# Kernel optimization log

Measured on AMD Instinct MI355X. Metric: run time of the kernel, lower is better.

Reference implementation:

```python
import jax, jax.numpy as jnp
import numpy as np

COMMIT = 0.25
DECAY = 0.999
EPS = 1e-05


def setup_inputs() -> dict:
    key = jax.random.key(0)
    k1, k2, k3, k4 = jax.random.split(key, 4)
    N, M, D = 8, 512, 32
    B, H, W = 32, 32, 32
    return {
        "x": jax.random.normal(k1, (B, N * D, H, W), jnp.float32),
        "embedding": jax.random.uniform(k2, (N, M, D), jnp.float32, -1.0 / M, 1.0 / M),
        "ema_count": jax.random.uniform(k3, (N, M), jnp.float32),
        "ema_weight": jax.random.normal(k4, (N, M, D), jnp.float32) * (1.0 / M),
    }


def reference(x, embedding, ema_count, ema_weight):
    B, C, H, W = x.shape
    N, M, D = embedding.shape  # C == N * D
    xr = x.reshape(B, N, D, H, W).transpose(1, 0, 3, 4, 2)  # [N,B,H,W,D]
    L = B * H * W
    x_flat = jax.lax.stop_gradient(xr).reshape(N, L, D)  # [N,L,D]

    e2 = jnp.sum(embedding ** 2, axis=2)[:, None, :]          # [N,1,M]
    x2 = jnp.sum(x_flat ** 2, axis=2, keepdims=True)          # [N,L,1]
    distances = e2 + x2 - 2.0 * jnp.einsum('nld,nmd->nlm', x_flat, embedding)

    indices = jnp.argmin(distances, axis=-1)                  # [N,L]
    quantized = jnp.take_along_axis(embedding, indices[:, :, None], axis=1)  # [N,L,D]
    quantized = jax.lax.stop_gradient(quantized).reshape(xr.shape)

    # one-hot count / encodings^T @ x_flat expressed as scatter-adds
    n_idx = jnp.arange(N)[:, None]
    counts = jnp.zeros((N, M), x.dtype).at[n_idx, indices].add(1.0)         # [N,M]
    dw = jnp.zeros((N, M, D), x.dtype).at[n_idx, indices].add(x_flat)       # [N,M,D]

    # EMA codebook update (training branch)
    ema_count_new = DECAY * ema_count + (1.0 - DECAY) * counts
    n_tot = jnp.sum(ema_count_new, axis=-1, keepdims=True)
    ema_count_new = (ema_count_new + EPS) / (n_tot + M * EPS) * n_tot
    ema_weight_new = DECAY * ema_weight + (1.0 - DECAY) * dw
    embedding_new = ema_weight_new / ema_count_new[..., None]

    e_latent_loss = jnp.mean((xr - quantized) ** 2)
    loss = COMMIT * e_latent_loss

    quantized_st = xr + jax.lax.stop_gradient(quantized - xr)  # straight-through
    out = quantized_st.transpose(1, 0, 4, 2, 3).reshape(B, C, H, W)

    avg_probs = counts / L                                     # mean of one-hot encodings
    perplexity = jnp.exp(-jnp.sum(avg_probs * jnp.log(avg_probs + 1e-10), axis=-1))

    return out, loss, perplexity.sum(), embedding_new, ema_count_new, ema_weight_new
```

## Files before the change

### kernel.cpp

```cpp
#include <hip/hip_runtime.h>
#include <cfloat>
#include <cmath>

#define NB 32
#define NN 8
#define NM 512
#define ND 32
#define NHW 1024
#define NC 256
#define NCHW (NC * NHW)
#define NL (NB * NHW)
#define EPAD 40
#define XPAD 33
#define TSTR (16 * EPAD)

static constexpr float DECAYF = (float)0.999;
static constexpr float OMDF = (float)(1.0 - 0.999);
static constexpr float EPSF = 1e-5f;
static constexpr float MEPSF = (float)(512.0 * 1e-5);
static constexpr float LOSS_SCALE = (float)(0.25 / 8388608.0);

#define OUT_LOSS (NB * NC * NHW)
#define OUT_PERP (OUT_LOSS + 1)
#define OUT_EMB (OUT_PERP + 1)
#define OUT_CNT (OUT_EMB + NN * NM * ND)
#define OUT_W (OUT_CNT + NN * NM)

typedef __attribute__((ext_vector_type(8))) short bf16x8;
typedef __attribute__((ext_vector_type(4))) float f32x4;

__device__ inline unsigned short f2bf(float f) {
    unsigned u = __builtin_bit_cast(unsigned, f);
    u += 0x7FFFu + ((u >> 16) & 1u);
    return (unsigned short)(u >> 16);
}
__device__ inline float bf2f(unsigned short h) {
    unsigned u = ((unsigned)h) << 16;
    return __builtin_bit_cast(float, u);
}

__global__ void e_prep(const float* __restrict__ emb, unsigned short* __restrict__ ehi,
                       unsigned short* __restrict__ elo, float* __restrict__ e2) {
    const int i = blockIdx.x * 256 + threadIdx.x;
    const float* e = emb + i * ND;
    unsigned short* hi = ehi + (size_t)i * EPAD;
    unsigned short* lo = elo + (size_t)i * EPAD;
    float s = 0.f;
#pragma unroll
    for (int d = 0; d < ND; ++d) {
        const float v = e[d];
        s = fmaf(v, v, s);
        const unsigned short h = f2bf(v);
        hi[d] = h;
        lo[d] = f2bf(v - bf2f(h));
    }
    e2[i] = s;
}

__launch_bounds__(256, 4)
__global__ void vq_argmin(const float* __restrict__ x,
                          const unsigned short* __restrict__ ehi,
                          const unsigned short* __restrict__ elo,
                          const float* __restrict__ e2g,
                          const float* __restrict__ emb,
                          float* __restrict__ out,
                          unsigned short* __restrict__ idx_out,
                          float* __restrict__ loss_out) {
    __shared__ __align__(16) float sx[256 * XPAD];
    __shared__ float se2[NM];
    __shared__ unsigned short sidx[256];
    __shared__ float red[4];

    const int n = blockIdx.y;
    const int lbase = blockIdx.x * 256;
    const int tid = threadIdx.x;
    const int b = lbase >> 10;
    const int hw0 = lbase & (NHW - 1);

    {
        const float* xp = x + (size_t)b * NCHW + n * ND * NHW + hw0 + tid;
#pragma unroll
        for (int d = 0; d < ND; ++d)
            sx[tid * XPAD + d] = xp[d * NHW];
    }
    for (int i = tid; i < NM; i += 256) se2[i] = e2g[n * NM + i];
    __syncthreads();

    const int lane = tid & 63;
    const int w = tid >> 6;
    const int j16 = lane & 15;
    const int kg = lane >> 4;

    bf16x8 ah[4], al[4];
#pragma unroll
    for (int lt = 0; lt < 4; ++lt) {
        const int row = w * 64 + lt * 16 + j16;
        const float* sr = &sx[row * XPAD + kg * 8];
#pragma unroll
        for (int j = 0; j < 8; ++j) {
            const float v = sr[j];
            const unsigned short h = f2bf(v);
            ah[lt][j] = (short)h;
            al[lt][j] = (short)f2bf(v - bf2f(h));
        }
    }

    float bd[4][4];
    int bm[4][4];
#pragma unroll
    for (int lt = 0; lt < 4; ++lt)
#pragma unroll
        for (int r = 0; r < 4; ++r) { bd[lt][r] = FLT_MAX; bm[lt][r] = 0; }

    const unsigned short* bh_base = ehi + ((size_t)n * NM + j16) * EPAD + kg * 8;
    const unsigned short* bl_base = elo + ((size_t)n * NM + j16) * EPAD + kg * 8;

    bf16x8 bh0 = *(const bf16x8*)(bh_base);
    bf16x8 bl0 = *(const bf16x8*)(bl_base);
    bf16x8 bh1 = *(const bf16x8*)(bh_base + TSTR);
    bf16x8 bl1 = *(const bf16x8*)(bl_base + TSTR);
    for (int mt = 0; mt < 32; mt += 2) {
        const bf16x8 cbh0 = bh0, cbl0 = bl0, cbh1 = bh1, cbl1 = bl1;
        if (mt < 30) {
            bh0 = *(const bf16x8*)(bh_base + (size_t)(mt + 2) * TSTR);
            bl0 = *(const bf16x8*)(bl_base + (size_t)(mt + 2) * TSTR);
            bh1 = *(const bf16x8*)(bh_base + (size_t)(mt + 3) * TSTR);
            bl1 = *(const bf16x8*)(bl_base + (size_t)(mt + 3) * TSTR);
        }
        {
            const int mloc = mt * 16 + j16;
            const float e2v = se2[mloc];
#pragma unroll
            for (int lt = 0; lt < 4; ++lt) {
                f32x4 c = {0.f, 0.f, 0.f, 0.f};
                c = __builtin_amdgcn_mfma_f32_16x16x32_bf16(ah[lt], cbh0, c, 0, 0, 0);
                c = __builtin_amdgcn_mfma_f32_16x16x32_bf16(al[lt], cbh0, c, 0, 0, 0);
                c = __builtin_amdgcn_mfma_f32_16x16x32_bf16(ah[lt], cbl0, c, 0, 0, 0);
#pragma unroll
                for (int r = 0; r < 4; ++r) {
                    const float dist = fmaf(-2.f, c[r], e2v);
                    if (dist < bd[lt][r]) { bd[lt][r] = dist; bm[lt][r] = mloc; }
                }
            }
        }
        {
            const int mloc = (mt + 1) * 16 + j16;
            const float e2v = se2[mloc];
#pragma unroll
            for (int lt = 0; lt < 4; ++lt) {
                f32x4 c = {0.f, 0.f, 0.f, 0.f};
                c = __builtin_amdgcn_mfma_f32_16x16x32_bf16(ah[lt], cbh1, c, 0, 0, 0);
                c = __builtin_amdgcn_mfma_f32_16x16x32_bf16(al[lt], cbh1, c, 0, 0, 0);
                c = __builtin_amdgcn_mfma_f32_16x16x32_bf16(ah[lt], cbl1, c, 0, 0, 0);
#pragma unroll
                for (int r = 0; r < 4; ++r) {
                    const float dist = fmaf(-2.f, c[r], e2v);
                    if (dist < bd[lt][r]) { bd[lt][r] = dist; bm[lt][r] = mloc; }
                }
            }
        }
    }

#pragma unroll
    for (int lt = 0; lt < 4; ++lt)
#pragma unroll
        for (int r = 0; r < 4; ++r) {
            float d0 = bd[lt][r];
            int m0 = bm[lt][r];
#pragma unroll
            for (int off = 1; off < 16; off <<= 1) {
                const float dn = __shfl_xor(d0, off, 64);
                const int mn = __shfl_xor(m0, off, 64);
                if (dn < d0 || (dn == d0 && mn < m0)) { d0 = dn; m0 = mn; }
            }
            bd[lt][r] = d0;
            bm[lt][r] = m0;
        }
    if (j16 == 0) {
#pragma unroll
        for (int lt = 0; lt < 4; ++lt)
#pragma unroll
            for (int r = 0; r < 4; ++r)
                sidx[w * 64 + lt * 16 + kg * 4 + r] = (unsigned short)bm[lt][r];
    }
    __syncthreads();

    const unsigned m = sidx[tid];
    idx_out[n * NL + lbase + tid] = (unsigned short)m;
    const float* q = emb + ((size_t)n * NM + m) * ND;
    float* op = out + (size_t)b * NCHW + n * ND * NHW + hw0 + tid;
    float lacc = 0.f;
#pragma unroll
    for (int d0 = 0; d0 < ND; d0 += 4) {
        const float4 qv = *(const float4*)&q[d0];
        float xd, df;
        xd = sx[tid * XPAD + d0 + 0]; op[(d0 + 0) * NHW] = qv.x; df = xd - qv.x; lacc = fmaf(df, df, lacc);
        xd = sx[tid * XPAD + d0 + 1]; op[(d0 + 1) * NHW] = qv.y; df = xd - qv.y; lacc = fmaf(df, df, lacc);
        xd = sx[tid * XPAD + d0 + 2]; op[(d0 + 2) * NHW] = qv.z; df = xd - qv.z; lacc = fmaf(df, df, lacc);
        xd = sx[tid * XPAD + d0 + 3]; op[(d0 + 3) * NHW] = qv.w; df = xd - qv.w; lacc = fmaf(df, df, lacc);
    }
#pragma unroll
    for (int off = 32; off; off >>= 1) lacc += __shfl_down(lacc, off);
    if (lane == 0) red[w] = lacc;
    __syncthreads();
    if (tid == 0)
        atomicAdd(loss_out, (red[0] + red[1] + red[2] + red[3]) * LOSS_SCALE);
}

__launch_bounds__(1024, 1)
__global__ void vq_scatter(const float* __restrict__ x,
                           const unsigned short* __restrict__ idx,
                           float* __restrict__ pdw, float* __restrict__ pcnt,
                           int bpc, int exclusive) {
    __shared__ float sdw[NM * XPAD];
    __shared__ float scnt[NM];
    const int n = blockIdx.y;
    const int ch = blockIdx.x;
    const int tid = threadIdx.x;

    for (int i = tid; i < NM * XPAD; i += 1024) sdw[i] = 0.f;
    if (tid < NM) scnt[tid] = 0.f;
    __syncthreads();

    for (int bb = 0; bb < bpc; ++bb) {
        const int b = ch * bpc + bb;
        const unsigned m = idx[n * NL + b * NHW + tid];
        const float* xp = x + (size_t)b * NCHW + n * ND * NHW;
        float* dst = &sdw[m * XPAD];
#pragma unroll
        for (int d = 0; d < ND; ++d)
            atomicAdd(&dst[d], xp[d * NHW + tid]);
        atomicAdd(&scnt[m], 1.0f);
    }
    __syncthreads();

    const int c = exclusive ? ch : 0;
    float* dwn = pdw + (size_t)c * (NN * NM * ND) + (size_t)n * NM * ND;
    if (exclusive) {
        for (int i = tid; i < NM * ND; i += 1024)
            dwn[i] = sdw[(i >> 5) * XPAD + (i & 31)];
        if (tid < NM) pcnt[(size_t)c * (NN * NM) + n * NM + tid] = scnt[tid];
    } else {
        for (int i = tid; i < NM * ND; i += 1024)
            atomicAdd(&dwn[i], sdw[(i >> 5) * XPAD + (i & 31)]);
        if (tid < NM) atomicAdd(&pcnt[n * NM + tid], scnt[tid]);
    }
}

__global__ void vq_update_cnt(const float* __restrict__ ema_count,
                              const float* __restrict__ pcnt,
                              float* __restrict__ out_cnt,
                              float* __restrict__ perp_out, int copies) {
    const int n = blockIdx.x;
    const int m = threadIdx.x;
    __shared__ float r1[8], r2[8];
    __shared__ float s_ntot;

    float cnt = 0.f;
    for (int c = 0; c < copies; ++c)
        cnt += pcnt[(size_t)c * (NN * NM) + n * NM + m];

    const float cnew = DECAYF * ema_count[n * NM + m] + OMDF * cnt;
    const float avg = cnt / (float)NL;
    const float pterm = avg * logf(avg + 1e-10f);

    float v1 = cnew, v2 = pterm;
#pragma unroll
    for (int off = 32; off; off >>= 1) {
        v1 += __shfl_down(v1, off);
        v2 += __shfl_down(v2, off);
    }
    if ((m & 63) == 0) { r1[m >> 6] = v1; r2[m >> 6] = v2; }
    __syncthreads();
    if (m == 0) {
        float a = 0.f, bsum = 0.f;
#pragma unroll
        for (int i = 0; i < 8; ++i) { a += r1[i]; bsum += r2[i]; }
        s_ntot = a;
        atomicAdd(perp_out, expf(-bsum));
    }
    __syncthreads();
    const float ntot = s_ntot;
    out_cnt[n * NM + m] = (cnew + EPSF) / (ntot + MEPSF) * ntot;
}

__global__ void vq_update_w(const float* __restrict__ ema_weight,
                            const float* __restrict__ pdw,
                            const float* __restrict__ out_cnt,
                            float* __restrict__ out_w,
                            float* __restrict__ out_emb, int copies) {
    const int i = blockIdx.x * 512 + threadIdx.x;
    float dw = 0.f;
    for (int c = 0; c < copies; ++c)
        dw += pdw[(size_t)c * (NN * NM * ND) + i];
    const float wnew = DECAYF * ema_weight[i] + OMDF * dw;
    out_w[i] = wnew;
    out_emb[i] = wnew / out_cnt[i >> 5];
}

extern "C" void kernel_launch(void* const* d_in, const int* in_sizes, int n_in,
                              void* d_out, int out_size, void* d_ws, size_t ws_size,
                              hipStream_t stream) {
    const float* x = (const float*)d_in[0];
    const float* emb = (const float*)d_in[1];
    const float* ema_count = (const float*)d_in[2];
    const float* ema_weight = (const float*)d_in[3];
    float* out = (float*)d_out;
    char* ws = (char*)d_ws;

    const size_t rest_bytes = 16384 + 327680 + 327680 + 524288;
    const size_t per_copy = (size_t)(NN * NM + NN * NM * ND) * 4;
    int copies, bpc;
    if (ws_size >= 16 * per_copy + rest_bytes)      { copies = 16; bpc = 2; }
    else if (ws_size >= 8 * per_copy + rest_bytes)  { copies = 8;  bpc = 4; }
    else                                            { copies = 1;  bpc = 4; }
    const int exclusive = (copies > 1) ? 1 : 0;

    float* pcnt = (float*)ws;
    float* pdw = (float*)(ws + (size_t)copies * NN * NM * 4);
    char* restp = ws + (size_t)copies * per_copy;
    float* e2 = (float*)restp;
    unsigned short* ehi = (unsigned short*)(restp + 16384);
    unsigned short* elo = (unsigned short*)(restp + 16384 + 327680);
    unsigned short* idxp = (unsigned short*)(restp + 16384 + 655360);

    if (!exclusive)
        hipMemsetAsync(ws, 0, per_copy, stream);
    hipMemsetAsync(out + OUT_LOSS, 0, 2 * sizeof(float), stream);

    e_prep<<<16, 256, 0, stream>>>(emb, ehi, elo, e2);
    vq_argmin<<<dim3(NL / 256, NN), 256, 0, stream>>>(x, ehi, elo, e2, emb, out, idxp,
                                                      out + OUT_LOSS);
    vq_scatter<<<dim3(NB / bpc, NN), 1024, 0, stream>>>(x, idxp, pdw, pcnt, bpc,
                                                        exclusive);
    vq_update_cnt<<<NN, NM, 0, stream>>>(ema_count, pcnt, out + OUT_CNT, out + OUT_PERP,
                                         copies);
    vq_update_w<<<NN * NM * ND / 512, 512, 0, stream>>>(ema_weight, pdw, out + OUT_CNT,
                                                        out + OUT_EMB, out + OUT_W, copies);
}
```

Baseline: 231.6 us.

## Stage x tiles in shared memory and spread scatter atomics across lanes

The scatter kernel now loads 128-position chunks of x with vectorized float4 reads, transposes them into padded shared memory, and has each warp lane own one dimension of a position. Atomic adds then go to distinct banks within a codebook row, instead of each thread issuing 32 serialized atomics to one row. Block size drops to 512 threads. When the workspace is large enough it uses 32 partial copies with one batch per block, which spreads the work over more blocks. The cost is extra barriers per chunk and more workspace for the final reduction.

```diff
diff --git a/kernel.cpp b/kernel.cpp
--- a/kernel.cpp
+++ b/kernel.cpp
@@ -13,6 +13,7 @@
 #define EPAD 40
 #define XPAD 33
 #define TSTR (16 * EPAD)
+#define SCHUNK 128
 
 static constexpr float DECAYF = (float)0.999;
 static constexpr float OMDF = (float)(1.0 - 0.999);
@@ -207,41 +208,64 @@
         atomicAdd(loss_out, (red[0] + red[1] + red[2] + red[3]) * LOSS_SCALE);
 }
 
-__launch_bounds__(1024, 1)
+__launch_bounds__(512, 1)
 __global__ void vq_scatter(const float* __restrict__ x,
                            const unsigned short* __restrict__ idx,
                            float* __restrict__ pdw, float* __restrict__ pcnt,
                            int bpc, int exclusive) {
     __shared__ float sdw[NM * XPAD];
     __shared__ float scnt[NM];
+    __shared__ float sx[SCHUNK * XPAD];
+    __shared__ unsigned short sm[SCHUNK];
     const int n = blockIdx.y;
     const int ch = blockIdx.x;
     const int tid = threadIdx.x;
 
-    for (int i = tid; i < NM * XPAD; i += 1024) sdw[i] = 0.f;
+    for (int i = tid; i < NM * XPAD; i += 512) sdw[i] = 0.f;
     if (tid < NM) scnt[tid] = 0.f;
     __syncthreads();
+
+    const int sd = tid >> 4;
+    const int si0 = (tid & 15) * 8;
+    const int ad = tid & 31;
+    const int apr = tid >> 5;
 
     for (int bb = 0; bb < bpc; ++bb) {
         const int b = ch * bpc + bb;
-        const unsigned m = idx[n * NL + b * NHW + tid];
         const float* xp = x + (size_t)b * NCHW + n * ND * NHW;
-        float* dst = &sdw[m * XPAD];
-#pragma unroll
-        for (int d = 0; d < ND; ++d)
-            atomicAdd(&dst[d], xp[d * NHW + tid]);
-        atomicAdd(&scnt[m], 1.0f);
-    }
-    __syncthreads();
+        const unsigned short* ip = idx + n * NL + b * NHW;
+        for (int c = 0; c < NHW / SCHUNK; ++c) {
+            {
+                const float* src = xp + sd * NHW + c * SCHUNK + si0;
+                const float4 v0 = *(const float4*)(src);
+                const float4 v1 = *(const float4*)(src + 4);
+                float* dst = &sx[si0 * XPAD + sd];
+                dst[0 * XPAD] = v0.x; dst[1 * XPAD] = v0.y;
+                dst[2 * XPAD] = v0.z; dst[3 * XPAD] = v0.w;
+                dst[4 * XPAD] = v1.x; dst[5 * XPAD] = v1.y;
+                dst[6 * XPAD] = v1.z; dst[7 * XPAD] = v1.w;
+            }
+            if (tid < SCHUNK) sm[tid] = ip[c * SCHUNK + tid];
+            __syncthreads();
+#pragma unroll
+            for (int it = 0; it < SCHUNK / 16; ++it) {
+                const int p = it * 16 + apr;
+                const unsigned m = sm[p];
+                atomicAdd(&sdw[m * XPAD + ad], sx[p * XPAD + ad]);
+                if (ad == 0) atomicAdd(&scnt[m], 1.0f);
+            }
+            __syncthreads();
+        }
+    }
 
     const int c = exclusive ? ch : 0;
     float* dwn = pdw + (size_t)c * (NN * NM * ND) + (size_t)n * NM * ND;
     if (exclusive) {
-        for (int i = tid; i < NM * ND; i += 1024)
+        for (int i = tid; i < NM * ND; i += 512)
             dwn[i] = sdw[(i >> 5) * XPAD + (i & 31)];
         if (tid < NM) pcnt[(size_t)c * (NN * NM) + n * NM + tid] = scnt[tid];
     } else {
-        for (int i = tid; i < NM * ND; i += 1024)
+        for (int i = tid; i < NM * ND; i += 512)
             atomicAdd(&dwn[i], sdw[(i >> 5) * XPAD + (i & 31)]);
         if (tid < NM) atomicAdd(&pcnt[n * NM + tid], scnt[tid]);
     }
@@ -311,7 +335,8 @@
     const size_t rest_bytes = 16384 + 327680 + 327680 + 524288;
     const size_t per_copy = (size_t)(NN * NM + NN * NM * ND) * 4;
     int copies, bpc;
-    if (ws_size >= 16 * per_copy + rest_bytes)      { copies = 16; bpc = 2; }
+    if (ws_size >= 32 * per_copy + rest_bytes)      { copies = 32; bpc = 1; }
+    else if (ws_size >= 16 * per_copy + rest_bytes) { copies = 16; bpc = 2; }
     else if (ws_size >= 8 * per_copy + rest_bytes)  { copies = 8;  bpc = 4; }
     else                                            { copies = 1;  bpc = 4; }
     const int exclusive = (copies > 1) ? 1 : 0;
@@ -331,8 +356,8 @@
     e_prep<<<16, 256, 0, stream>>>(emb, ehi, elo, e2);
     vq_argmin<<<dim3(NL / 256, NN), 256, 0, stream>>>(x, ehi, elo, e2, emb, out, idxp,
                                                       out + OUT_LOSS);
-    vq_scatter<<<dim3(NB / bpc, NN), 1024, 0, stream>>>(x, idxp, pdw, pcnt, bpc,
-                                                        exclusive);
+    vq_scatter<<<dim3(NB / bpc, NN), 512, 0, stream>>>(x, idxp, pdw, pcnt, bpc,
+                                                       exclusive);
     vq_update_cnt<<<NN, NM, 0, stream>>>(ema_count, pcnt, out + OUT_CNT, out + OUT_PERP,
                                          copies);
     vq_update_w<<<NN * NM * ND / 512, 512, 0, stream>>>(ema_weight, pdw, out + OUT_CNT,
```

Measured after the change: 205.7 us. 11.2% less time.
